# Kernel optimization log

Measured on AMD Instinct MI355X. Metric: run time of the kernel, lower is better.

## Reference

```python
import jax, jax.numpy as jnp
import numpy as np

EPS = 1e-12  # matches torch F.normalize default eps

def setup_inputs() -> dict:
    key = jax.random.key(0)
    k1, k2 = jax.random.split(key)
    query = jax.random.normal(k1, (8, 2048, 512), dtype=jnp.float32)
    support = jax.random.normal(k2, (8, 4096, 512), dtype=jnp.float32)
    return {"query": query, "support": support}

def _l2_normalize(x):
    # torch.nn.functional.normalize(x, dim=-1): x / max(||x||, eps)
    n = jnp.sqrt(jnp.sum(x * x, axis=-1, keepdims=True))
    return x / jnp.maximum(n, EPS)

def reference(query, support):
    # cosine distance: 1 - q_hat @ s_hat^T  -> [B, Nq, Ns]
    qn = _l2_normalize(query)
    sn = _l2_normalize(support)
    dist = 1.0 - jnp.einsum('bqd,bsd->bqs', qn, sn)
    min_d = jnp.min(dist, axis=2)        # [B, Nq]
    return jnp.mean(min_d, axis=1)       # [B]
```

## Files before the change

### kernel.cpp

```cpp
#include <hip/hip_runtime.h>
#include <hip/hip_bf16.h>

typedef __attribute__((ext_vector_type(8))) short short8;
typedef __attribute__((ext_vector_type(4))) float f32x4;
typedef __attribute__((ext_vector_type(16))) float f32x16;
typedef __attribute__((ext_vector_type(8))) int int8v;

#define D   512
#define NQ  2048
#define NS  4096
#define NB  8
#define BM  128
#define BN  128
#define BK  32

typedef const __attribute__((address_space(1))) unsigned int gas_uint;
typedef __attribute__((address_space(3))) unsigned int las_uint;

#define WAIT_VM8   0x0F78
#define WAIT_VM0   0x0F70
#define WAIT_LGKM0 0xC07F

__device__ __forceinline__ short f2bf(float f) {
  unsigned u = __builtin_bit_cast(unsigned, f);
  unsigned r = u + 0x7fffu + ((u >> 16) & 1u);
  return (short)(r >> 16);
}

__device__ __forceinline__ short8 pack8(float4 a, float4 b, float r) {
  short8 o;
  o[0] = f2bf(a.x * r); o[1] = f2bf(a.y * r); o[2] = f2bf(a.z * r); o[3] = f2bf(a.w * r);
  o[4] = f2bf(b.x * r); o[5] = f2bf(b.y * r); o[6] = f2bf(b.z * r); o[7] = f2bf(b.w * r);
  return o;
}

__global__ void normcvt8_kernel(const float* __restrict__ q, const float* __restrict__ s,
                                unsigned char* __restrict__ qn, unsigned char* __restrict__ sn,
                                unsigned* __restrict__ maxenc) {
  if (blockIdx.x < 64) maxenc[(blockIdx.x << 8) | threadIdx.x] = 0;
  int wave = blockIdx.x * 4 + (threadIdx.x >> 6);
  int lane = threadIdx.x & 63;
  const int NQR = NB * NQ;
  const float4* src; unsigned char* dst;
  if (wave < NQR) { src = (const float4*)(q + (size_t)wave * D); dst = qn + (size_t)wave * D; }
  else {
    size_t w = wave - NQR;
    src = (const float4*)(s + w * D); dst = sn + w * D;
  }
  float4 a = src[lane * 2];
  float4 b = src[lane * 2 + 1];
  float ss = a.x*a.x + a.y*a.y + a.z*a.z + a.w*a.w
           + b.x*b.x + b.y*b.y + b.z*b.z + b.w*b.w;
  #pragma unroll
  for (int m = 32; m >= 1; m >>= 1) ss += __shfl_xor(ss, m, 64);
  float r = 1.0f / fmaxf(sqrtf(ss), 1e-12f);
  int w0 = __builtin_amdgcn_cvt_pk_fp8_f32(a.x * r, a.y * r, 0, false);
  w0     = __builtin_amdgcn_cvt_pk_fp8_f32(a.z * r, a.w * r, w0, true);
  int w1 = __builtin_amdgcn_cvt_pk_fp8_f32(b.x * r, b.y * r, 0, false);
  w1     = __builtin_amdgcn_cvt_pk_fp8_f32(b.z * r, b.w * r, w1, true);
  *(int2*)(dst + lane * 8) = make_int2(w0, w1);
}

__global__ __launch_bounds__(256, 2) void cosmax14_kernel(
    const unsigned char* __restrict__ Qn, const unsigned char* __restrict__ Sn,
    unsigned int* __restrict__ maxenc)
{
  __shared__ __align__(16) unsigned char sbuf[65536];
  __shared__ float maxbuf[64][4];

  const int id  = blockIdx.x;
  const int b   = id & 7;
  const int j   = id >> 3;
  const int mt  = j & 31;
  const int nsp = j >> 5;
  const int tid  = threadIdx.x;
  const int wave = tid >> 6;
  const int lane = tid & 63;
  const int l31 = lane & 31, kc = lane >> 5;

  {
    const unsigned char* Qbase = Qn + ((size_t)b * NQ + (size_t)mt * 64) * D;
    const int baserow = wave * 2 + (lane >> 5);
    #pragma unroll
    for (int p = 0; p < 8; ++p) {
      int row = p * 8 + baserow;
      int g   = (lane & 31) ^ (row & 31);
      __builtin_amdgcn_global_load_lds(
          (gas_uint*)(Qbase + (size_t)row * D + g * 16),
          (las_uint*)(sbuf + 16384 + p * 4096 + wave * 1024), 16, 0, 0);
    }
  }
  __syncthreads();

  const int srow8 = lane >> 3;
  const int sch   = (lane & 7) ^ srow8;
  const unsigned char* gS = Sn +
      ((size_t)b * NS + (size_t)nsp * 2048 + wave * 32 + srow8) * D + sch * 16;

  auto issue = [&](size_t goff, int ldsoff) {
    #pragma unroll
    for (int t = 0; t < 4; ++t)
      __builtin_amdgcn_global_load_lds((gas_uint*)(gS + goff + (size_t)t * 4096),
          (las_uint*)(sbuf + ldsoff + wave * 4096 + t * 1024), 16, 0, 0);
  };

  issue(0, 0);

  int8v a[2][8];
  #pragma unroll
  for (int m = 0; m < 2; ++m) {
    const int arow = m * 32 + l31;
    #pragma unroll
    for (int kk = 0; kk < 8; ++kk) {
      int c0 = (4 * kk + 2 * kc) ^ l31;
      ((int4*)&a[m][kk])[0] = *(const int4*)&sbuf[16384 + arow * 512 + c0 * 16];
      ((int4*)&a[m][kk])[1] = *(const int4*)&sbuf[16384 + arow * 512 + (c0 ^ 1) * 16];
    }
  }
  __builtin_amdgcn_s_waitcnt(WAIT_LGKM0);
  asm volatile("" ::: "memory");
  __builtin_amdgcn_s_barrier();
  asm volatile("" ::: "memory");
  issue(128, 16384);
  issue(256, 32768);
  issue(384, 49152);

  const int brow = (wave * 32 + l31) * 128;
  const int cxor = ((kc * 2) ^ (l31 & 7)) * 16;

  f32x16 acc0, acc1;
  float rmax0[16], rmax1[16];
  #pragma unroll
  for (int r = 0; r < 16; ++r) { rmax0[r] = -2.0f; rmax1[r] = -2.0f; }

  auto computeK = [&](int kt, int rdo) {
    const unsigned char* Bb = sbuf + rdo;
    #pragma unroll
    for (int ss = 0; ss < 2; ++ss) {
      const int cb = cxor ^ (ss * 64);
      int8v b0;
      ((int4*)&b0)[0] = *(const int4*)&Bb[brow + cb];
      ((int4*)&b0)[1] = *(const int4*)&Bb[brow + (cb ^ 16)];
      acc0 = __builtin_amdgcn_mfma_scale_f32_32x32x64_f8f6f4(
          a[0][kt * 2 + ss], b0, acc0, 0, 0, 0, 0x7f7f7f7f, 0, 0x7f7f7f7f);
      acc1 = __builtin_amdgcn_mfma_scale_f32_32x32x64_f8f6f4(
          a[1][kt * 2 + ss], b0, acc1, 0, 0, 0, 0x7f7f7f7f, 0, 0x7f7f7f7f);
    }
  };

  #pragma clang loop unroll(disable)
  for (int nt2 = 0; nt2 < 16; ++nt2) {
    const size_t ntb = (size_t)nt2 << 16;
    const bool more = (nt2 < 15);

    if (nt2 == 0) __builtin_amdgcn_s_waitcnt(WAIT_VM8);
    else          __builtin_amdgcn_s_waitcnt(WAIT_VM0);
    asm volatile("" ::: "memory");
    __builtin_amdgcn_s_barrier();
    asm volatile("" ::: "memory");
    if (nt2 > 0) {
      issue(ntb + 256, 32768);
      issue(ntb + 384, 49152);
    }
    #pragma unroll
    for (int r = 0; r < 16; ++r) { acc0[r] = 0.f; acc1[r] = 0.f; }
    computeK(0, 0);
    computeK(1, 16384);

    __builtin_amdgcn_s_waitcnt(WAIT_VM0);
    asm volatile("" ::: "memory");
    __builtin_amdgcn_s_barrier();
    asm volatile("" ::: "memory");
    if (more) {
      issue(ntb + 65536, 0);
      issue(ntb + 65536 + 128, 16384);
    }
    computeK(2, 32768);
    computeK(3, 49152);

    #pragma unroll
    for (int r = 0; r < 16; ++r) {
      rmax0[r] = fmaxf(rmax0[r], acc0[r]);
      rmax1[r] = fmaxf(rmax1[r], acc1[r]);
    }
  }

  #pragma unroll
  for (int m = 0; m < 2; ++m) {
    #pragma unroll
    for (int r = 0; r < 16; ++r) {
      float v = m ? rmax1[r] : rmax0[r];
      v = fmaxf(v, __shfl_xor(v, 1, 64));
      v = fmaxf(v, __shfl_xor(v, 2, 64));
      v = fmaxf(v, __shfl_xor(v, 4, 64));
      v = fmaxf(v, __shfl_xor(v, 8, 64));
      v = fmaxf(v, __shfl_xor(v, 16, 64));
      if (l31 == 0)
        maxbuf[m * 32 + (r & 3) + 8 * (r >> 2) + 4 * kc][wave] = v;
    }
  }
  __syncthreads();

  if (tid < 64) {
    float v = fmaxf(fmaxf(maxbuf[tid][0], maxbuf[tid][1]),
                    fmaxf(maxbuf[tid][2], maxbuf[tid][3]));
    unsigned e = __builtin_bit_cast(unsigned, v);
    e = ((int)e >= 0) ? (e | 0x80000000u) : ~e;
    atomicMax(&maxenc[(size_t)b * NQ + (size_t)mt * 64 + tid], e);
  }
}

__global__ void finalize_kernel(const unsigned* __restrict__ maxenc,
                                float* __restrict__ out) {
  int b = blockIdx.x;
  int tid = threadIdx.x;
  float sum = 0.f;
  for (int i = tid; i < NQ; i += 256) {
    unsigned e = maxenc[(size_t)b * NQ + i];
    unsigned u = (e & 0x80000000u) ? (e & 0x7fffffffu) : ~e;
    float v = __builtin_bit_cast(float, u);
    sum += 1.0f - v;
  }
  #pragma unroll
  for (int m = 32; m >= 1; m >>= 1) sum += __shfl_xor(sum, m, 64);
  __shared__ float part[4];
  if ((tid & 63) == 0) part[tid >> 6] = sum;
  __syncthreads();
  if (tid == 0) out[b] = (part[0] + part[1] + part[2] + part[3]) * (1.0f / (float)NQ);
}

__global__ void norms_kernel(const float* __restrict__ q, const float* __restrict__ s,
                             float* __restrict__ rq, float* __restrict__ rs) {
  int wave = blockIdx.x * 4 + (threadIdx.x >> 6);
  int lane = threadIdx.x & 63;
  const int NQR = NB * NQ, NSR = NB * NS;
  if (wave >= NQR + NSR) return;
  const float4* r4; float* outp;
  if (wave < NQR) { r4 = (const float4*)(q + (size_t)wave * D); outp = rq + wave; }
  else           { r4 = (const float4*)(s + (size_t)(wave - NQR) * D); outp = rs + (wave - NQR); }
  float4 a = r4[lane];
  float4 b = r4[lane + 64];
  float ss = a.x*a.x + a.y*a.y + a.z*a.z + a.w*a.w
           + b.x*b.x + b.y*b.y + b.z*b.z + b.w*b.w;
  #pragma unroll
  for (int m = 32; m >= 1; m >>= 1) ss += __shfl_xor(ss, m, 64);
  if (lane == 0) *outp = 1.0f / fmaxf(sqrtf(ss), 1e-12f);
}

__global__ __launch_bounds__(256, 3) void cosmax_kernel(
    const float* __restrict__ Q, const float* __restrict__ S,
    const float* __restrict__ rq, const float* __restrict__ rs,
    unsigned int* __restrict__ maxenc)
{
  __shared__ short As[BM * BK];
  __shared__ short Bs[BN * BK];
  __shared__ float maxbuf[BM][2];

  const int b  = blockIdx.z, mt = blockIdx.y, nt = blockIdx.x;
  const float* Qb  = Q + ((size_t)b * NQ + mt * BM) * D;
  const float* Sb  = S + ((size_t)b * NS + nt * BN) * D;
  const float* rqb = rq + (size_t)b * NQ + mt * BM;
  const float* rsb = rs + (size_t)b * NS + nt * BN;

  const int tid  = threadIdx.x;
  const int srow = tid >> 2;
  const int kseg = (tid & 3) * 8;
  const float rq0 = rqb[srow], rq1 = rqb[srow + 64];
  const float rs0 = rsb[srow], rs1 = rsb[srow + 64];
  const int wave = tid >> 6, lane = tid & 63;
  const int wm = (wave & 1) * 64, wn = (wave >> 1) * 64;
  const int lm = lane & 15, lk = (lane >> 4) * 8;

  f32x4 acc[4][4];
  #pragma unroll
  for (int i = 0; i < 4; ++i)
    #pragma unroll
    for (int j = 0; j < 4; ++j) acc[i][j] = (f32x4){0.f, 0.f, 0.f, 0.f};

  const float* qrow0 = Qb + (size_t)srow * D + kseg;
  const float* qrow1 = qrow0 + (size_t)64 * D;
  const float* srow0 = Sb + (size_t)srow * D + kseg;
  const float* srow1 = srow0 + (size_t)64 * D;

  float4 qa, qb2, qc, qd, sa, sb2, sc, sd;
  #define LOADK(k0)                                                    \
    qa  = *(const float4*)(qrow0 + (k0));  qb2 = *(const float4*)(qrow0 + (k0) + 4); \
    qc  = *(const float4*)(qrow1 + (k0));  qd  = *(const float4*)(qrow1 + (k0) + 4); \
    sa  = *(const float4*)(srow0 + (k0));  sb2 = *(const float4*)(srow0 + (k0) + 4); \
    sc  = *(const float4*)(srow1 + (k0));  sd  = *(const float4*)(srow1 + (k0) + 4);
  LOADK(0);
  #pragma unroll 4
  for (int kt = 0; kt < D / BK; ++kt) {
    *(short8*)&As[srow        * BK + kseg] = pack8(qa, qb2, rq0);
    *(short8*)&As[(srow + 64) * BK + kseg] = pack8(qc, qd,  rq1);
    *(short8*)&Bs[srow        * BK + kseg] = pack8(sa, sb2, rs0);
    *(short8*)&Bs[(srow + 64) * BK + kseg] = pack8(sc, sd,  rs1);
    __syncthreads();
    if (kt < D / BK - 1) { LOADK((kt + 1) * BK); }
    short8 af[4], bf[4];
    #pragma unroll
    for (int i = 0; i < 4; ++i) af[i] = *(short8*)&As[(wm + i * 16 + lm) * BK + lk];
    #pragma unroll
    for (int j = 0; j < 4; ++j) bf[j] = *(short8*)&Bs[(wn + j * 16 + lm) * BK + lk];
    #pragma unroll
    for (int i = 0; i < 4; ++i)
      #pragma unroll
      for (int j = 0; j < 4; ++j)
        acc[i][j] = __builtin_amdgcn_mfma_f32_16x16x32_bf16(af[i], bf[j], acc[i][j], 0, 0, 0);
    __syncthreads();
  }
  #undef LOADK

  #pragma unroll
  for (int i = 0; i < 4; ++i) {
    #pragma unroll
    for (int r = 0; r < 4; ++r) {
      float v = fmaxf(fmaxf(acc[i][0][r], acc[i][1][r]),
                      fmaxf(acc[i][2][r], acc[i][3][r]));
      v = fmaxf(v, __shfl_xor(v, 1, 64));
      v = fmaxf(v, __shfl_xor(v, 2, 64));
      v = fmaxf(v, __shfl_xor(v, 4, 64));
      v = fmaxf(v, __shfl_xor(v, 8, 64));
      if ((lane & 15) == 0) {
        int row = wm + i * 16 + (lane >> 4) * 4 + r;
        maxbuf[row][wave >> 1] = v;
      }
    }
  }
  __syncthreads();
  if (tid < BM) {
    float v = fmaxf(maxbuf[tid][0], maxbuf[tid][1]);
    unsigned e = __builtin_bit_cast(unsigned, v);
    e = ((int)e >= 0) ? (e | 0x80000000u) : ~e;
    atomicMax(&maxenc[(size_t)b * NQ + mt * BM + tid], e);
  }
}

extern "C" void kernel_launch(void* const* d_in, const int* in_sizes, int n_in,
                              void* d_out, int out_size, void* d_ws, size_t ws_size,
                              hipStream_t stream) {
  const float* q = (const float*)d_in[0];
  const float* s = (const float*)d_in[1];
  float* out = (float*)d_out;

  unsigned* maxenc = (unsigned*)d_ws;
  const size_t QOFF = 65536;
  const size_t SOFF = QOFF + (size_t)NB * NQ * D;
  const size_t NEED = SOFF + (size_t)NB * NS * D;

  if (ws_size >= NEED) {
    unsigned char* qn = (unsigned char*)d_ws + QOFF;
    unsigned char* sn = (unsigned char*)d_ws + SOFF;
    normcvt8_kernel<<<NB * (NQ + NS) / 4, 256, 0, stream>>>(q, s, qn, sn, maxenc);
    cosmax14_kernel<<<512, 256, 0, stream>>>(qn, sn, maxenc);
    finalize_kernel<<<NB, 256, 0, stream>>>(maxenc, out);
  } else {
    float* rq = (float*)((char*)d_ws + 65536);
    float* rs = (float*)((char*)d_ws + 131072);
    hipMemsetAsync(maxenc, 0, (size_t)NB * NQ * sizeof(unsigned), stream);
    norms_kernel<<<NB * (NQ + NS) / 4, 256, 0, stream>>>(q, s, rq, rs);
    dim3 grid(NS / BN, NQ / BM, NB);
    cosmax_kernel<<<grid, 256, 0, stream>>>(q, s, rq, rs, maxenc);
    finalize_kernel<<<NB, 256, 0, stream>>>(maxenc, out);
  }
}
```

Baseline: 167.1 us.

## Replace barrier-synchronised double-stage pipeline with per-chunk vmcnt-staged prefetch

The main loop now refills each 16 KB LDS chunk as soon as it has been consumed, instead of refilling in two halves guarded by workgroup barriers. Readiness is checked with graduated vmcnt waits, which keeps three chunk loads in flight and removes the s_barrier calls. This only holds if each wave reads back only the LDS rows it loaded itself. The inner MFMA group is also unrolled, with both B fragments loaded up front and the MFMA block wrapped in s_setprio to favour issuing matrix instructions.

```diff
diff --git a/kernel.cpp b/kernel.cpp
--- a/kernel.cpp
+++ b/kernel.cpp
@@ -17,7 +17,9 @@
 typedef const __attribute__((address_space(1))) unsigned int gas_uint;
 typedef __attribute__((address_space(3))) unsigned int las_uint;
 
+#define WAIT_VM12  0x0F7C
 #define WAIT_VM8   0x0F78
+#define WAIT_VM4   0x0F74
 #define WAIT_VM0   0x0F70
 #define WAIT_LGKM0 0xC07F
 
@@ -61,7 +63,7 @@
   *(int2*)(dst + lane * 8) = make_int2(w0, w1);
 }
 
-__global__ __launch_bounds__(256, 2) void cosmax14_kernel(
+__global__ __launch_bounds__(256, 2) void cosmax15_kernel(
     const unsigned char* __restrict__ Qn, const unsigned char* __restrict__ Sn,
     unsigned int* __restrict__ maxenc)
 {
@@ -123,10 +125,10 @@
   asm volatile("" ::: "memory");
   issue(128, 16384);
   issue(256, 32768);
-  issue(384, 49152);
 
   const int brow = (wave * 32 + l31) * 128;
-  const int cxor = ((kc * 2) ^ (l31 & 7)) * 16;
+  const int cb0  = ((kc * 2) ^ (l31 & 7)) * 16;
+  const int cb1  = cb0 ^ 64;
 
   f32x16 acc0, acc1;
   float rmax0[16], rmax1[16];
@@ -135,47 +137,50 @@
 
   auto computeK = [&](int kt, int rdo) {
     const unsigned char* Bb = sbuf + rdo;
-    #pragma unroll
-    for (int ss = 0; ss < 2; ++ss) {
-      const int cb = cxor ^ (ss * 64);
-      int8v b0;
-      ((int4*)&b0)[0] = *(const int4*)&Bb[brow + cb];
-      ((int4*)&b0)[1] = *(const int4*)&Bb[brow + (cb ^ 16)];
-      acc0 = __builtin_amdgcn_mfma_scale_f32_32x32x64_f8f6f4(
-          a[0][kt * 2 + ss], b0, acc0, 0, 0, 0, 0x7f7f7f7f, 0, 0x7f7f7f7f);
-      acc1 = __builtin_amdgcn_mfma_scale_f32_32x32x64_f8f6f4(
-          a[1][kt * 2 + ss], b0, acc1, 0, 0, 0, 0x7f7f7f7f, 0, 0x7f7f7f7f);
-    }
+    int8v b0, b1;
+    ((int4*)&b0)[0] = *(const int4*)&Bb[brow + cb0];
+    ((int4*)&b0)[1] = *(const int4*)&Bb[brow + (cb0 ^ 16)];
+    ((int4*)&b1)[0] = *(const int4*)&Bb[brow + cb1];
+    ((int4*)&b1)[1] = *(const int4*)&Bb[brow + (cb1 ^ 16)];
+    __builtin_amdgcn_s_setprio(1);
+    acc0 = __builtin_amdgcn_mfma_scale_f32_32x32x64_f8f6f4(
+        a[0][kt * 2], b0, acc0, 0, 0, 0, 0x7f7f7f7f, 0, 0x7f7f7f7f);
+    acc1 = __builtin_amdgcn_mfma_scale_f32_32x32x64_f8f6f4(
+        a[1][kt * 2], b0, acc1, 0, 0, 0, 0x7f7f7f7f, 0, 0x7f7f7f7f);
+    acc0 = __builtin_amdgcn_mfma_scale_f32_32x32x64_f8f6f4(
+        a[0][kt * 2 + 1], b1, acc0, 0, 0, 0, 0x7f7f7f7f, 0, 0x7f7f7f7f);
+    acc1 = __builtin_amdgcn_mfma_scale_f32_32x32x64_f8f6f4(
+        a[1][kt * 2 + 1], b1, acc1, 0, 0, 0, 0x7f7f7f7f, 0, 0x7f7f7f7f);
+    __builtin_amdgcn_s_setprio(0);
   };
+
+  #define KSTEP(WAITIMM)                       \
+    asm volatile("" ::: "memory");             \
+    __builtin_amdgcn_s_waitcnt(WAITIMM);       \
+    asm volatile("" ::: "memory");
 
   #pragma clang loop unroll(disable)
   for (int nt2 = 0; nt2 < 16; ++nt2) {
     const size_t ntb = (size_t)nt2 << 16;
     const bool more = (nt2 < 15);
 
-    if (nt2 == 0) __builtin_amdgcn_s_waitcnt(WAIT_VM8);
-    else          __builtin_amdgcn_s_waitcnt(WAIT_VM0);
-    asm volatile("" ::: "memory");
-    __builtin_amdgcn_s_barrier();
-    asm volatile("" ::: "memory");
-    if (nt2 > 0) {
-      issue(ntb + 256, 32768);
-      issue(ntb + 384, 49152);
-    }
     #pragma unroll
     for (int r = 0; r < 16; ++r) { acc0[r] = 0.f; acc1[r] = 0.f; }
+
+    issue(ntb + 384, 49152);
+    KSTEP(WAIT_VM12);
     computeK(0, 0);
+
+    if (more) { issue(ntb + 65536, 0); KSTEP(WAIT_VM12); }
+    else      { KSTEP(WAIT_VM8); }
     computeK(1, 16384);
 
-    __builtin_amdgcn_s_waitcnt(WAIT_VM0);
-    asm volatile("" ::: "memory");
-    __builtin_amdgcn_s_barrier();
-    asm volatile("" ::: "memory");
-    if (more) {
-      issue(ntb + 65536, 0);
-      issue(ntb + 65536 + 128, 16384);
-    }
+    if (more) { issue(ntb + 65536 + 128, 16384); KSTEP(WAIT_VM12); }
+    else      { KSTEP(WAIT_VM4); }
     computeK(2, 32768);
+
+    if (more) { issue(ntb + 65536 + 256, 32768); KSTEP(WAIT_VM12); }
+    else      { KSTEP(WAIT_VM0); }
     computeK(3, 49152);
 
     #pragma unroll
@@ -184,6 +189,7 @@
       rmax1[r] = fmaxf(rmax1[r], acc1[r]);
     }
   }
+  #undef KSTEP
 
   #pragma unroll
   for (int m = 0; m < 2; ++m) {
@@ -352,7 +358,7 @@
     unsigned char* qn = (unsigned char*)d_ws + QOFF;
     unsigned char* sn = (unsigned char*)d_ws + SOFF;
     normcvt8_kernel<<<NB * (NQ + NS) / 4, 256, 0, stream>>>(q, s, qn, sn, maxenc);
-    cosmax14_kernel<<<512, 256, 0, stream>>>(qn, sn, maxenc);
+    cosmax15_kernel<<<512, 256, 0, stream>>>(qn, sn, maxenc);
     finalize_kernel<<<NB, 256, 0, stream>>>(maxenc, out);
   } else {
     float* rq = (float*)((char*)d_ws + 65536);
```

Measured after the change: 160.0 us, median of 2. 1.04x faster.
